# Optimization experiments

Hardware: AMD Instinct MI355X
Metric: run time of the kernel (lower is better)

## Reference

```python
import jax, jax.numpy as jnp
import numpy as np
import math

D_MODEL = 1024
NUM_HEADS = 16
D_K = D_MODEL // NUM_HEADS
MAX_LEN = 2048
B, S = 2, 1024


def setup_inputs() -> dict:
    key = jax.random.key(0)
    ks = jax.random.split(key, 10)
    lin_scale = 1.0 / math.sqrt(D_MODEL)
    # torch Linear: weight (out, in), y = x @ W.T + b
    Wq = jax.random.uniform(ks[0], (D_MODEL, D_MODEL), jnp.float32, -lin_scale, lin_scale)
    Wk = jax.random.uniform(ks[1], (D_MODEL, D_MODEL), jnp.float32, -lin_scale, lin_scale)
    Wv = jax.random.uniform(ks[2], (D_MODEL, D_MODEL), jnp.float32, -lin_scale, lin_scale)
    Wo = jax.random.uniform(ks[3], (D_MODEL, D_MODEL), jnp.float32, -lin_scale, lin_scale)
    bq = jnp.zeros((D_MODEL,), jnp.float32)
    bk = jnp.zeros((D_MODEL,), jnp.float32)
    bv = jnp.zeros((D_MODEL,), jnp.float32)
    bo = jnp.zeros((D_MODEL,), jnp.float32)
    # xavier_uniform for Er (max_len, d_k)
    er_bound = math.sqrt(6.0 / (MAX_LEN + D_K))
    Er = jax.random.uniform(ks[4], (MAX_LEN, D_K), jnp.float32, -er_bound, er_bound)
    x = jax.random.normal(ks[5], (B, S, D_MODEL), jnp.float32)
    return {"x": x, "Wq": Wq, "bq": bq, "Wk": Wk, "bk": bk,
            "Wv": Wv, "bv": bv, "Wo": Wo, "bo": bo, "Er": Er}


def reference(x, Wq, bq, Wk, bk, Wv, bv, Wo, bo, Er):
    Bsz, Slen, Dm = x.shape
    H, dk = NUM_HEADS, D_K

    def proj(W, b):
        y = jnp.einsum('bsd,ed->bse', x, W) + b
        return y.reshape(Bsz, Slen, H, dk).transpose(0, 2, 1, 3)  # (B,H,S,dk)

    Q = proj(Wq, bq)
    K = proj(Wk, bk)
    V = proj(Wv, bv)

    # content-content scores
    AC = jnp.einsum('bhid,bhjd->bhij', Q, K)  # (B,H,S,S)

    # relative position embeddings for distances S-1 .. -(S-1)
    rel_pos = jnp.arange(Slen - 1, -Slen, -1)  # (2S-1,)
    idx = rel_pos + (Slen - 1)                 # map to 0..2S-2 (requires 2S-1 <= max_len)
    Er_emb = Er[idx]                           # (2S-1, dk)
    BD_full = jnp.einsum('bhid,md->bhim', Q, Er_emb)  # (B,H,S,2S-1)

    # relative shift: final[i,j] = BD_full[i, S-1 - i + j] (column for distance i-j)
    i_idx = jnp.arange(Slen)[:, None]                  # (S,1)
    m_idx = (Slen - 1) - i_idx + jnp.arange(Slen)[None, :]  # (S,S)
    BD = BD_full[:, :, i_idx, m_idx]                   # (B,H,S,S)

    scores = (AC + BD) / math.sqrt(dk)
    attn = jax.nn.softmax(scores, axis=-1)  # dropout is identity at eval
    out = jnp.einsum('bhij,bhjd->bhid', attn, V)       # (B,H,S,dk)
    out = out.transpose(0, 2, 1, 3).reshape(Bsz, Slen, Dm)
    return jnp.einsum('bsd,ed->bse', out, Wo) + bo
```

## Files before the change

kernel.cpp:

```cpp
#include <hip/hip_runtime.h>
#include <hip/hip_bf16.h>
#include <math.h>

#define D_MODEL 1024
#define NUM_HEADS 16
#define D_K 64
#define SEQ 1024
#define BATCH 2

typedef __hip_bfloat16 bf16;
typedef __bf16 bf16x8 __attribute__((ext_vector_type(8)));
typedef __bf16 bf16x4 __attribute__((ext_vector_type(4)));
typedef float floatx4 __attribute__((ext_vector_type(4)));

__device__ __forceinline__ floatx4 mfma16(bf16x8 a, bf16x8 b, floatx4 c) {
    return __builtin_amdgcn_mfma_f32_16x16x32_bf16(a, b, c, 0, 0, 0);
}

__device__ __forceinline__ void gl_lds16(const bf16* g, __bf16* l) {
    __builtin_amdgcn_global_load_lds(
        (const __attribute__((address_space(1))) void*)g,
        (__attribute__((address_space(3))) void*)l, 16, 0, 0);
}

__global__ void detect_dtype_kernel(const void* __restrict__ x, int* __restrict__ flag) {
    __shared__ int cnt[256];
    const float* xf = (const float*)x;
    const int tid = threadIdx.x;
    int sane = 0;
    for (int i = tid; i < 4096; i += 256) {
        float v = xf[i];
        float a = fabsf(v);
        if (v == 0.0f || (a > 1e-8f && a < 1e8f)) sane++;
    }
    cnt[tid] = sane;
    __syncthreads();
    for (int s = 128; s > 0; s >>= 1) {
        if (tid < s) cnt[tid] += cnt[tid + s];
        __syncthreads();
    }
    if (tid == 0) flag[0] = (cnt[0] > 3686) ? 1 : 0;
}

struct ConvSrcs { const void* p[10]; };

__global__ __launch_bounds__(256) void convert_all_kernel(ConvSrcs srcs,
                                                          bf16* __restrict__ dstbase,
                                                          const int* __restrict__ flag) {
    const long long e = ((long long)blockIdx.x * 256 + threadIdx.x) * 8;
    int seg; long long base;
    if      (e < 2097152LL) { seg = 0; base = 0; }
    else if (e < 3145728LL) { seg = 1; base = 2097152LL; }
    else if (e < 4194304LL) { seg = 2; base = 3145728LL; }
    else if (e < 5242880LL) { seg = 3; base = 4194304LL; }
    else if (e < 6291456LL) { seg = 4; base = 5242880LL; }
    else if (e < 6292480LL) { seg = 5; base = 6291456LL; }
    else if (e < 6293504LL) { seg = 6; base = 6292480LL; }
    else if (e < 6294528LL) { seg = 7; base = 6293504LL; }
    else if (e < 6295552LL) { seg = 8; base = 6294528LL; }
    else                    { seg = 9; base = 6295552LL; }
    const long long local = e - base;
    __bf16 tmp[8];
    if (*flag) {
        const float* s = (const float*)srcs.p[seg] + local;
#pragma unroll
        for (int t = 0; t < 8; ++t) tmp[t] = (__bf16)s[t];
        *(bf16x8*)(void*)(dstbase + e) = *(const bf16x8*)tmp;
    } else {
        *(bf16x8*)(void*)(dstbase + e) =
            *(const bf16x8*)(const void*)((const bf16*)srcs.p[seg] + local);
    }
}

__global__ __launch_bounds__(256) void gemm_qkv_kernel(const bf16* __restrict__ x,
        const bf16* __restrict__ Wq, const bf16* __restrict__ Wk, const bf16* __restrict__ Wv,
        const bf16* __restrict__ bq, const bf16* __restrict__ bk, const bf16* __restrict__ bv,
        bf16* __restrict__ Qb, bf16* __restrict__ Kb, bf16* __restrict__ Vt) {
    const int wsel = blockIdx.x >> 4;
    const int n0 = (blockIdx.x & 15) * 64;
    const int m0 = blockIdx.y * 128;
    const bf16* W    = (wsel == 0) ? Wq : ((wsel == 1) ? Wk : Wv);
    const bf16* bias = (wsel == 0) ? bq : ((wsel == 1) ? bk : bv);

    __shared__ __bf16 smem[128 * 128 + 64 * 128];
    __bf16* As = smem;
    __bf16* Bs = smem + 16384;

    const int tid = threadIdx.x;
    const int wave = tid >> 6, lane = tid & 63, quad = lane >> 4, l16 = lane & 15;
    const int wr = (wave >> 1) * 64, wc = (wave & 1) * 32;
    const int lrow = lane >> 4;
    const int lcg  = lane & 15;

    floatx4 acc[4][2];
#pragma unroll
    for (int r = 0; r < 4; ++r)
#pragma unroll
        for (int c = 0; c < 2; ++c) acc[r][c] = (floatx4)0.f;

    for (int k0 = 0; k0 < 1024; k0 += 128) {
        __syncthreads();
#pragma unroll
        for (int i = 0; i < 8; ++i) {
            const int ci = wave * 8 + i;
            const int grow = ci * 4 + lrow;
            const int gcg = lcg ^ (grow & 15);
            gl_lds16(x + (size_t)(m0 + grow) * 1024 + k0 + gcg * 8, As + ci * 512);
        }
#pragma unroll
        for (int i = 0; i < 4; ++i) {
            const int ci = wave * 4 + i;
            const int grow = ci * 4 + lrow;
            const int gcg = lcg ^ (grow & 15);
            gl_lds16(W + (size_t)(n0 + grow) * 1024 + k0 + gcg * 8, Bs + ci * 512);
        }
        __syncthreads();
#pragma unroll
        for (int kk = 0; kk < 4; ++kk) {
            bf16x8 af[4], bfr[2];
#pragma unroll
            for (int r = 0; r < 4; ++r) {
                const int row = wr + r * 16 + l16;
                const int sg = (kk * 4 + quad) ^ l16;
                af[r] = *(const bf16x8*)&As[row * 128 + sg * 8];
            }
#pragma unroll
            for (int c = 0; c < 2; ++c) {
                const int row = wc + c * 16 + l16;
                const int sg = (kk * 4 + quad) ^ l16;
                bfr[c] = *(const bf16x8*)&Bs[row * 128 + sg * 8];
            }
#pragma unroll
            for (int r = 0; r < 4; ++r)
#pragma unroll
                for (int c = 0; c < 2; ++c)
                    acc[r][c] = mfma16(af[r], bfr[c], acc[r][c]);
        }
    }

    if (wsel < 2) {
        bf16* Cb = (wsel == 0) ? Qb : Kb;
#pragma unroll
        for (int c = 0; c < 2; ++c) {
            const int col = n0 + wc + c * 16 + l16;
            const float bvl = (float)bias[col];
#pragma unroll
            for (int r = 0; r < 4; ++r)
#pragma unroll
                for (int v = 0; v < 4; ++v) {
                    const int row = m0 + wr + r * 16 + quad * 4 + v;
                    Cb[(size_t)row * 1024 + col] = (bf16)(acc[r][c][v] + bvl);
                }
        }
    } else {
        __bf16* Ls = smem;
        __syncthreads();
#pragma unroll
        for (int c = 0; c < 2; ++c) {
            const int col = wc + c * 16 + l16;
            const float bvl = (float)bias[n0 + col];
#pragma unroll
            for (int r = 0; r < 4; ++r)
#pragma unroll
                for (int v = 0; v < 4; ++v) {
                    const int row = wr + r * 16 + quad * 4 + v;
                    Ls[col * 132 + row] = (__bf16)(acc[r][c][v] + bvl);
                }
        }
        __syncthreads();
        const int b = m0 >> 10, s0 = m0 & 1023, h = n0 >> 6;
        const int d = tid >> 2, sg2 = (tid & 3) * 32;
        bf16* g = Vt + ((size_t)((b * NUM_HEADS + h) * 64 + d)) * SEQ + s0 + sg2;
#pragma unroll
        for (int c = 0; c < 32; c += 8)
            *(bf16x8*)(void*)(g + c) = *(const bf16x8*)&Ls[d * 132 + sg2 + c];
    }
}

__global__ __launch_bounds__(256, 3) void attn_mfma_kernel(const bf16* __restrict__ Q,
                                                           const bf16* __restrict__ Kc,
                                                           const bf16* __restrict__ Vt,
                                                           const bf16* __restrict__ Er,
                                                           bf16* __restrict__ Opart,
                                                           float* __restrict__ Ml) {
    const int i0 = blockIdx.x * 128;
    const int h = blockIdx.y;
    const int zz = blockIdx.z;
    const int b = zz / 3, jsel = zz - b * 3;
    const int tid = threadIdx.x;
    const int wave = tid >> 6, lane = tid & 63, quad = lane >> 4, l16 = lane & 15;

    const int jbeg = (jsel == 0) ? 0 : ((jsel == 1) ? 384 : 704);
    const int nt   = (jsel == 0) ? 6 : 5;

    __shared__ __bf16 Ks[64][72];
    __shared__ __bf16 Vs[80][72];
    __shared__ __bf16 scr_all[4][3264];
    __bf16* scr = &scr_all[wave][0];
    __bf16* Qs = &scr_all[0][0];

    for (int e = tid; e < 16 * 72; e += 256) {
        const int r = e / 72, c = e - r * 72;
        Vs[64 + r][c] = (r == 0) ? (__bf16)1.0f : (__bf16)0.0f;
    }
    {
        const int r = tid >> 1, cg = (tid & 1) * 32;
        const bf16* g = Q + ((size_t)(b * SEQ + i0 + r)) * D_MODEL + h * 64 + cg;
#pragma unroll
        for (int c = 0; c < 32; c += 8)
            *(bf16x8*)(void*)(Qs + r * 72 + cg + c) = *(const bf16x8*)(const void*)(g + c);
    }
    __syncthreads();
    bf16x8 aq[2][2];
#pragma unroll
    for (int half = 0; half < 2; ++half)
#pragma unroll
        for (int kk = 0; kk < 2; ++kk)
            aq[half][kk] = *(const bf16x8*)(const void*)(
                Qs + (wave * 32 + half * 16 + l16) * 72 + kk * 32 + quad * 8);

    floatx4 oacc[5][2];
#pragma unroll
    for (int ct = 0; ct < 5; ++ct)
#pragma unroll
        for (int half = 0; half < 2; ++half) oacc[ct][half] = (floatx4)0.f;

    const int eb = 960 + i0;
    const bf16* Kg = Kc + (size_t)b * SEQ * D_MODEL + h * 64;
    const bf16* Vtg = Vt + (size_t)((b * NUM_HEADS + h) * 64) * SEQ;

    const int r4 = tid >> 2, c4 = (tid & 3) * 16;
    bf16x8 kp0, kp1, vp0, vp1;
    {
        const bf16* kg = Kg + (size_t)(jbeg + r4) * D_MODEL + c4;
        const bf16* vg = Vtg + (size_t)r4 * SEQ + jbeg + c4;
        kp0 = *(const bf16x8*)(const void*)kg;
        kp1 = *(const bf16x8*)(const void*)(kg + 8);
        vp0 = *(const bf16x8*)(const void*)vg;
        vp1 = *(const bf16x8*)(const void*)(vg + 8);
    }

    for (int t = 0; t < nt; ++t) {
        const int j0 = jbeg + t * 64;
        __syncthreads();
        *(bf16x8*)&Ks[r4][c4]     = kp0;
        *(bf16x8*)&Ks[r4][c4 + 8] = kp1;
        *(bf16x8*)&Vs[r4][c4]     = vp0;
        *(bf16x8*)&Vs[r4][c4 + 8] = vp1;
        __syncthreads();
        if (t < nt - 1) {
            const int jn = j0 + 64;
            const bf16* kg = Kg + (size_t)(jn + r4) * D_MODEL + c4;
            const bf16* vg = Vtg + (size_t)r4 * SEQ + jn + c4;
            kp0 = *(const bf16x8*)(const void*)kg;
            kp1 = *(const bf16x8*)(const void*)(kg + 8);
            vp0 = *(const bf16x8*)(const void*)vg;
            vp1 = *(const bf16x8*)(const void*)(vg + 8);
        }

#pragma unroll
        for (int ct = 0; ct < 6; ++ct) {
            const int erow = eb - j0 + wave * 32 + ct * 16 + l16;
            const bf16* ep = Er + (size_t)erow * 64 + quad * 8;
            bf16x8 be0 = *(const bf16x8*)(const void*)ep;
            bf16x8 be1 = *(const bf16x8*)(const void*)(ep + 32);
#pragma unroll
            for (int half = 0; half < 2; ++half) {
                floatx4 tv = (floatx4)0.f;
                tv = mfma16(aq[half][0], be0, tv);
                tv = mfma16(aq[half][1], be1, tv);
                bf16x4 tb;
#pragma unroll
                for (int v = 0; v < 4; ++v) tb[v] = (__bf16)tv[v];
                *(bf16x4*)(void*)(scr + (ct * 16 + l16) * 34 + half * 16 + quad * 4) = tb;
            }
        }
        floatx4 sfrag[4][2];
#pragma unroll
        for (int ct = 0; ct < 4; ++ct) {
            bf16x8 bk0 = *(const bf16x8*)&Ks[ct * 16 + l16][quad * 8];
            bf16x8 bk1 = *(const bf16x8*)&Ks[ct * 16 + l16][32 + quad * 8];
#pragma unroll
            for (int half = 0; half < 2; ++half) {
                floatx4 s = (floatx4)0.f;
                s = mfma16(aq[half][0], bk0, s);
                s = mfma16(aq[half][1], bk1, s);
                sfrag[ct][half] = s;
            }
        }
#pragma unroll
        for (int ct = 0; ct < 4; ++ct)
#pragma unroll
            for (int half = 0; half < 2; ++half)
#pragma unroll
                for (int v = 0; v < 4; ++v) {
                    const int rl = half * 16 + quad * 4 + v;
                    const int cl = 63 + rl - (ct * 16 + l16);
                    sfrag[ct][half][v] =
                        (sfrag[ct][half][v] + (float)scr[cl * 34 + rl]) * 0.125f;
                }
#pragma unroll
        for (int ct = 0; ct < 4; ++ct)
#pragma unroll
            for (int half = 0; half < 2; ++half)
#pragma unroll
                for (int v = 0; v < 4; ++v) {
                    const int rl = half * 16 + quad * 4 + v;
                    scr[rl * 72 + ct * 16 + l16] = (__bf16)__expf(sfrag[ct][half][v]);
                }
        bf16x8 ap[2][2];
#pragma unroll
        for (int half = 0; half < 2; ++half)
#pragma unroll
            for (int kk = 0; kk < 2; ++kk)
                ap[half][kk] = *(const bf16x8*)(const void*)(
                    scr + (half * 16 + l16) * 72 + kk * 32 + quad * 8);
#pragma unroll
        for (int ct = 0; ct < 5; ++ct) {
            bf16x8 bv0 = *(const bf16x8*)&Vs[ct * 16 + l16][quad * 8];
            bf16x8 bv1 = *(const bf16x8*)&Vs[ct * 16 + l16][32 + quad * 8];
#pragma unroll
            for (int half = 0; half < 2; ++half) {
                oacc[ct][half] = mfma16(ap[half][0], bv0, oacc[ct][half]);
                oacc[ct][half] = mfma16(ap[half][1], bv1, oacc[ct][half]);
            }
        }
    }

    bf16* Op = Opart + (size_t)jsel * 2097152;
#pragma unroll
    for (int ct = 0; ct < 4; ++ct)
#pragma unroll
        for (int half = 0; half < 2; ++half)
#pragma unroll
            for (int v = 0; v < 4; ++v) {
                const int row = i0 + wave * 32 + half * 16 + quad * 4 + v;
                const int col = h * 64 + ct * 16 + l16;
                Op[((size_t)(b * SEQ + row)) * D_MODEL + col] = (bf16)oacc[ct][half][v];
            }
    if (l16 == 0) {
        const int base = ((jsel * 2 + b) * 16 + h) * 1024;
#pragma unroll
        for (int half = 0; half < 2; ++half)
#pragma unroll
            for (int v = 0; v < 4; ++v) {
                const int ig = i0 + wave * 32 + half * 16 + quad * 4 + v;
                Ml[base + ig] = oacc[4][half][v];
            }
    }
}

__global__ __launch_bounds__(256) void combine_kernel(const bf16* __restrict__ Opart,
                                                      const float* __restrict__ Ml,
                                                      bf16* __restrict__ Ob) {
    const int e = (blockIdx.x * 256 + threadIdx.x) * 8;
    const int row = e >> 10;
    const int b = row >> 10, i = row & 1023;
    const int h = (e & 1023) >> 6;
    float l = 0.f;
#pragma unroll
    for (int s = 0; s < 3; ++s) l += Ml[(((s * 2 + b) * 16 + h) << 10) + i];
    const float inv = 1.0f / l;
    bf16x8 o1 = *(const bf16x8*)(const void*)(Opart + e);
    bf16x8 o2 = *(const bf16x8*)(const void*)(Opart + 2097152 + e);
    bf16x8 o3 = *(const bf16x8*)(const void*)(Opart + 4194304 + e);
    bf16x8 o;
#pragma unroll
    for (int v = 0; v < 8; ++v)
        o[v] = (__bf16)(((float)o1[v] + (float)o2[v] + (float)o3[v]) * inv);
    *(bf16x8*)(void*)(Ob + e) = o;
}

__global__ __launch_bounds__(256) void gemm_out_kernel(const bf16* __restrict__ A,
        const bf16* __restrict__ W, const bf16* __restrict__ bias,
        void* __restrict__ C, const int* __restrict__ flag) {
    const int n0 = blockIdx.x * 64;
    const int m0 = blockIdx.y * 64;
    __shared__ __bf16 smem[64 * 128 * 2];
    __bf16* As = smem;
    __bf16* Bs = smem + 8192;
    const int tid = threadIdx.x;
    const int wave = tid >> 6, lane = tid & 63, quad = lane >> 4, l16 = lane & 15;
    const int wr = (wave >> 1) * 32, wc = (wave & 1) * 32;
    const int lrow = lane >> 4, lcg = lane & 15;

    floatx4 acc[2][2];
#pragma unroll
    for (int r = 0; r < 2; ++r)
#pragma unroll
        for (int c = 0; c < 2; ++c) acc[r][c] = (floatx4)0.f;

    for (int k0 = 0; k0 < 1024; k0 += 128) {
        __syncthreads();
#pragma unroll
        for (int i = 0; i < 4; ++i) {
            const int ci = wave * 4 + i;
            const int grow = ci * 4 + lrow;
            const int gcg = lcg ^ (grow & 15);
            gl_lds16(A + (size_t)(m0 + grow) * 1024 + k0 + gcg * 8, As + ci * 512);
            gl_lds16(W + (size_t)(n0 + grow) * 1024 + k0 + gcg * 8, Bs + ci * 512);
        }
        __syncthreads();
#pragma unroll
        for (int kk = 0; kk < 4; ++kk) {
            bf16x8 af[2], bfr[2];
            const int sg = (kk * 4 + quad) ^ l16;
#pragma unroll
            for (int r = 0; r < 2; ++r)
                af[r] = *(const bf16x8*)&As[(wr + r * 16 + l16) * 128 + sg * 8];
#pragma unroll
            for (int c = 0; c < 2; ++c)
                bfr[c] = *(const bf16x8*)&Bs[(wc + c * 16 + l16) * 128 + sg * 8];
#pragma unroll
            for (int r = 0; r < 2; ++r)
#pragma unroll
                for (int c = 0; c < 2; ++c)
                    acc[r][c] = mfma16(af[r], bfr[c], acc[r][c]);
        }
    }
#pragma unroll
    for (int c = 0; c < 2; ++c) {
        const int col = n0 + wc + c * 16 + l16;
        const float bvl = (float)bias[col];
#pragma unroll
        for (int r = 0; r < 2; ++r)
#pragma unroll
            for (int v = 0; v < 4; ++v) {
                const int row = m0 + wr + r * 16 + quad * 4 + v;
                const float val = acc[r][c][v] + bvl;
                const size_t idx = (size_t)row * 1024 + col;
                if (*flag) ((float*)C)[idx] = val;
                else       ((bf16*)C)[idx] = (bf16)val;
            }
    }
}

extern "C" void kernel_launch(void* const* d_in, const int* in_sizes, int n_in,
                              void* d_out, int out_size, void* d_ws, size_t ws_size,
                              hipStream_t stream) {
    const size_t E_X = 2097152;
    const size_t E_CANON = 6426624;

    char* ws = (char*)d_ws;
    int* flag = (int*)ws;
    bf16* canon = (bf16*)(ws + 16);
    bf16* xc  = canon;
    bf16* Wqc = canon + 2097152;
    bf16* Wkc = canon + 3145728;
    bf16* Wvc = canon + 4194304;
    bf16* Woc = canon + 5242880;
    bf16* bqc = canon + 6291456;
    bf16* bkc = canon + 6292480;
    bf16* bvc = canon + 6293504;
    bf16* boc = canon + 6294528;
    bf16* Erc = canon + 6295552;
    bf16* p = canon + E_CANON;
    bf16* Qb    = p;  p += E_X;
    bf16* Kb    = p;  p += E_X;
    bf16* Vt    = p;  p += E_X;
    bf16* Opart = p;  p += 3 * E_X;
    float* Ml   = (float*)p;

    detect_dtype_kernel<<<1, 256, 0, stream>>>(d_in[0], flag);

    ConvSrcs cs;
    cs.p[0] = d_in[0]; cs.p[1] = d_in[1]; cs.p[2] = d_in[3]; cs.p[3] = d_in[5];
    cs.p[4] = d_in[7]; cs.p[5] = d_in[2]; cs.p[6] = d_in[4]; cs.p[7] = d_in[6];
    cs.p[8] = d_in[8]; cs.p[9] = d_in[9];
    convert_all_kernel<<<3138, 256, 0, stream>>>(cs, canon, flag);

    gemm_qkv_kernel<<<dim3(48, 16), 256, 0, stream>>>(xc, Wqc, Wkc, Wvc,
                                                      bqc, bkc, bvc, Qb, Kb, Vt);

    attn_mfma_kernel<<<dim3(8, 16, 6), 256, 0, stream>>>(Qb, Kb, Vt, Erc, Opart, Ml);

    combine_kernel<<<1024, 256, 0, stream>>>(Opart, Ml, Qb);

    gemm_out_kernel<<<dim3(16, 32), 256, 0, stream>>>(Qb, Woc, boc, d_out, flag);
}
```

Measured before the change: 177.8 us.

## Fuse dtype detection into convert kernel and widen QKV GEMM tile to 128x128

The separate single-block dtype-detection kernel is folded into the conversion kernel. Every block now recomputes the sanity check on the first 1024 floats of x and uses the result locally, and block 0 still writes the flag for later kernels. This removes one launch and one serialized dependency, at the cost of a shared-memory reduction with barriers in every convert block. The QKV projection GEMM goes from 128x64 to 128x128 output tiles, with 4x4 MFMA accumulators per wave and the V-transpose epilogue rewritten to match. That raises data reuse per LDS load but halves the grid to 384 blocks, which may underfill the GPU.

```diff
diff --git a/kernel.cpp b/kernel.cpp
--- a/kernel.cpp
+++ b/kernel.cpp
@@ -23,31 +23,33 @@
         (__attribute__((address_space(3))) void*)l, 16, 0, 0);
 }
 
-__global__ void detect_dtype_kernel(const void* __restrict__ x, int* __restrict__ flag) {
+struct ConvSrcs { const void* p[10]; };
+
+__global__ __launch_bounds__(256) void convert_all_kernel(ConvSrcs srcs,
+                                                          bf16* __restrict__ dstbase,
+                                                          int* __restrict__ flagg) {
     __shared__ int cnt[256];
-    const float* xf = (const float*)x;
     const int tid = threadIdx.x;
-    int sane = 0;
-    for (int i = tid; i < 4096; i += 256) {
-        float v = xf[i];
-        float a = fabsf(v);
-        if (v == 0.0f || (a > 1e-8f && a < 1e8f)) sane++;
-    }
-    cnt[tid] = sane;
+    {
+        const float* xf = (const float*)srcs.p[0];
+        int sane = 0;
+#pragma unroll
+        for (int i = 0; i < 4; ++i) {
+            const float v = xf[tid * 4 + i];
+            const float a = fabsf(v);
+            if (v == 0.0f || (a > 1e-8f && a < 1e8f)) sane++;
+        }
+        cnt[tid] = sane;
+    }
     __syncthreads();
     for (int s = 128; s > 0; s >>= 1) {
         if (tid < s) cnt[tid] += cnt[tid + s];
         __syncthreads();
     }
-    if (tid == 0) flag[0] = (cnt[0] > 3686) ? 1 : 0;
-}
-
-struct ConvSrcs { const void* p[10]; };
-
-__global__ __launch_bounds__(256) void convert_all_kernel(ConvSrcs srcs,
-                                                          bf16* __restrict__ dstbase,
-                                                          const int* __restrict__ flag) {
-    const long long e = ((long long)blockIdx.x * 256 + threadIdx.x) * 8;
+    const int flag = (cnt[0] > 922) ? 1 : 0;
+    if (blockIdx.x == 0 && tid == 0) flagg[0] = flag;
+
+    const long long e = ((long long)blockIdx.x * 256 + tid) * 8;
     int seg; long long base;
     if      (e < 2097152LL) { seg = 0; base = 0; }
     else if (e < 3145728LL) { seg = 1; base = 2097152LL; }
@@ -61,7 +63,7 @@
     else                    { seg = 9; base = 6295552LL; }
     const long long local = e - base;
     __bf16 tmp[8];
-    if (*flag) {
+    if (flag) {
         const float* s = (const float*)srcs.p[seg] + local;
 #pragma unroll
         for (int t = 0; t < 8; ++t) tmp[t] = (__bf16)s[t];
@@ -72,31 +74,31 @@
     }
 }
 
-__global__ __launch_bounds__(256) void gemm_qkv_kernel(const bf16* __restrict__ x,
+__global__ __launch_bounds__(256, 2) void gemm_qkv_kernel(const bf16* __restrict__ x,
         const bf16* __restrict__ Wq, const bf16* __restrict__ Wk, const bf16* __restrict__ Wv,
         const bf16* __restrict__ bq, const bf16* __restrict__ bk, const bf16* __restrict__ bv,
         bf16* __restrict__ Qb, bf16* __restrict__ Kb, bf16* __restrict__ Vt) {
-    const int wsel = blockIdx.x >> 4;
-    const int n0 = (blockIdx.x & 15) * 64;
+    const int wsel = blockIdx.x >> 3;
+    const int n0 = (blockIdx.x & 7) * 128;
     const int m0 = blockIdx.y * 128;
     const bf16* W    = (wsel == 0) ? Wq : ((wsel == 1) ? Wk : Wv);
     const bf16* bias = (wsel == 0) ? bq : ((wsel == 1) ? bk : bv);
 
-    __shared__ __bf16 smem[128 * 128 + 64 * 128];
+    __shared__ __bf16 smem[128 * 128 * 2];
     __bf16* As = smem;
     __bf16* Bs = smem + 16384;
 
     const int tid = threadIdx.x;
     const int wave = tid >> 6, lane = tid & 63, quad = lane >> 4, l16 = lane & 15;
-    const int wr = (wave >> 1) * 64, wc = (wave & 1) * 32;
+    const int wr = (wave >> 1) * 64, wc = (wave & 1) * 64;
     const int lrow = lane >> 4;
     const int lcg  = lane & 15;
 
-    floatx4 acc[4][2];
+    floatx4 acc[4][4];
 #pragma unroll
     for (int r = 0; r < 4; ++r)
 #pragma unroll
-        for (int c = 0; c < 2; ++c) acc[r][c] = (floatx4)0.f;
+        for (int c = 0; c < 4; ++c) acc[r][c] = (floatx4)0.f;
 
     for (int k0 = 0; k0 < 1024; k0 += 128) {
         __syncthreads();
@@ -106,34 +108,23 @@
             const int grow = ci * 4 + lrow;
             const int gcg = lcg ^ (grow & 15);
             gl_lds16(x + (size_t)(m0 + grow) * 1024 + k0 + gcg * 8, As + ci * 512);
-        }
-#pragma unroll
-        for (int i = 0; i < 4; ++i) {
-            const int ci = wave * 4 + i;
-            const int grow = ci * 4 + lrow;
-            const int gcg = lcg ^ (grow & 15);
             gl_lds16(W + (size_t)(n0 + grow) * 1024 + k0 + gcg * 8, Bs + ci * 512);
         }
         __syncthreads();
 #pragma unroll
         for (int kk = 0; kk < 4; ++kk) {
-            bf16x8 af[4], bfr[2];
-#pragma unroll
-            for (int r = 0; r < 4; ++r) {
-                const int row = wr + r * 16 + l16;
-                const int sg = (kk * 4 + quad) ^ l16;
-                af[r] = *(const bf16x8*)&As[row * 128 + sg * 8];
-            }
-#pragma unroll
-            for (int c = 0; c < 2; ++c) {
-                const int row = wc + c * 16 + l16;
-                const int sg = (kk * 4 + quad) ^ l16;
-                bfr[c] = *(const bf16x8*)&Bs[row * 128 + sg * 8];
-            }
+            const int sg = ((kk * 4 + quad) ^ l16) * 8;
+            bf16x8 af[4], bfr[4];
 #pragma unroll
             for (int r = 0; r < 4; ++r)
-#pragma unroll
-                for (int c = 0; c < 2; ++c)
+                af[r] = *(const bf16x8*)&As[(wr + r * 16 + l16) * 128 + sg];
+#pragma unroll
+            for (int c = 0; c < 4; ++c)
+                bfr[c] = *(const bf16x8*)&Bs[(wc + c * 16 + l16) * 128 + sg];
+#pragma unroll
+            for (int r = 0; r < 4; ++r)
+#pragma unroll
+                for (int c = 0; c < 4; ++c)
                     acc[r][c] = mfma16(af[r], bfr[c], acc[r][c]);
         }
     }
@@ -141,7 +132,7 @@
     if (wsel < 2) {
         bf16* Cb = (wsel == 0) ? Qb : Kb;
 #pragma unroll
-        for (int c = 0; c < 2; ++c) {
+        for (int c = 0; c < 4; ++c) {
             const int col = n0 + wc + c * 16 + l16;
             const float bvl = (float)bias[col];
 #pragma unroll
@@ -156,7 +147,7 @@
         __bf16* Ls = smem;
         __syncthreads();
 #pragma unroll
-        for (int c = 0; c < 2; ++c) {
+        for (int c = 0; c < 4; ++c) {
             const int col = wc + c * 16 + l16;
             const float bvl = (float)bias[n0 + col];
 #pragma unroll
@@ -168,11 +159,12 @@
                 }
         }
         __syncthreads();
-        const int b = m0 >> 10, s0 = m0 & 1023, h = n0 >> 6;
-        const int d = tid >> 2, sg2 = (tid & 3) * 32;
-        bf16* g = Vt + ((size_t)((b * NUM_HEADS + h) * 64 + d)) * SEQ + s0 + sg2;
-#pragma unroll
-        for (int c = 0; c < 32; c += 8)
+        const int b = m0 >> 10, s0 = m0 & 1023, h0 = n0 >> 6;
+        const int d = tid >> 1, sg2 = (tid & 1) * 64;
+        bf16* g = Vt + ((size_t)((b * NUM_HEADS + h0 + (d >> 6)) * 64 + (d & 63))) * SEQ
+                  + s0 + sg2;
+#pragma unroll
+        for (int c = 0; c < 64; c += 8)
             *(bf16x8*)(void*)(g + c) = *(const bf16x8*)&Ls[d * 132 + sg2 + c];
     }
 }
@@ -404,13 +396,13 @@
 #pragma unroll
         for (int kk = 0; kk < 4; ++kk) {
             bf16x8 af[2], bfr[2];
-            const int sg = (kk * 4 + quad) ^ l16;
+            const int sg = ((kk * 4 + quad) ^ l16) * 8;
 #pragma unroll
             for (int r = 0; r < 2; ++r)
-                af[r] = *(const bf16x8*)&As[(wr + r * 16 + l16) * 128 + sg * 8];
+                af[r] = *(const bf16x8*)&As[(wr + r * 16 + l16) * 128 + sg];
 #pragma unroll
             for (int c = 0; c < 2; ++c)
-                bfr[c] = *(const bf16x8*)&Bs[(wc + c * 16 + l16) * 128 + sg * 8];
+                bfr[c] = *(const bf16x8*)&Bs[(wc + c * 16 + l16) * 128 + sg];
 #pragma unroll
             for (int r = 0; r < 2; ++r)
 #pragma unroll
@@ -461,15 +453,13 @@
     bf16* Opart = p;  p += 3 * E_X;
     float* Ml   = (float*)p;
 
-    detect_dtype_kernel<<<1, 256, 0, stream>>>(d_in[0], flag);
-
     ConvSrcs cs;
     cs.p[0] = d_in[0]; cs.p[1] = d_in[1]; cs.p[2] = d_in[3]; cs.p[3] = d_in[5];
     cs.p[4] = d_in[7]; cs.p[5] = d_in[2]; cs.p[6] = d_in[4]; cs.p[7] = d_in[6];
     cs.p[8] = d_in[8]; cs.p[9] = d_in[9];
     convert_all_kernel<<<3138, 256, 0, stream>>>(cs, canon, flag);
 
-    gemm_qkv_kernel<<<dim3(48, 16), 256, 0, stream>>>(xc, Wqc, Wkc, Wvc,
+    gemm_qkv_kernel<<<dim3(24, 16), 256, 0, stream>>>(xc, Wqc, Wkc, Wvc,
                                                       bqc, bkc, bvc, Qb, Kb, Vt);
 
     attn_mfma_kernel<<<dim3(8, 16, 6), 256, 0, stream>>>(Qb, Kb, Vt, Erc, Opart, Ml);
```

Result: no change. 177.7 us (median of 3 runs) (-0.1%).
